# Performance work log

Hardware: AMD Instinct MI355X
Metric: run time of the kernel (lower is better)

## Reference

```python
import jax, jax.numpy as jnp
import numpy as np

GROUPS = 32
EPS = 1e-5


def setup_inputs() -> dict:
    key = jax.random.key(0)
    ks = jax.random.split(key, 8)
    B, C, H, W = 4, 512, 64, 64
    s = 1.0 / np.sqrt(C)  # conv1x1 fan-in init scale
    return {
        "x": jax.random.normal(ks[0], (B, C, H, W), dtype=jnp.float32),
        "gn_gamma": jnp.ones((C,), dtype=jnp.float32),
        "gn_beta": jnp.zeros((C,), dtype=jnp.float32),
        "wq": jax.random.normal(ks[1], (C, C), dtype=jnp.float32) * s,
        "bq": jnp.zeros((C,), dtype=jnp.float32),
        "wk": jax.random.normal(ks[2], (C, C), dtype=jnp.float32) * s,
        "bk": jnp.zeros((C,), dtype=jnp.float32),
        "wv": jax.random.normal(ks[3], (C, C), dtype=jnp.float32) * s,
        "bv": jnp.zeros((C,), dtype=jnp.float32),
    }


def reference(x, gn_gamma, gn_beta, wq, bq, wk, bk, wv, bv):
    B, C, H, W = x.shape
    N = H * W
    # GroupNorm over (channels-within-group, H, W)
    xg = x.reshape(B, GROUPS, C // GROUPS, H, W)
    mean = xg.mean(axis=(2, 3, 4), keepdims=True)
    var = xg.var(axis=(2, 3, 4), keepdims=True)
    xn = ((xg - mean) * jax.lax.rsqrt(var + EPS)).reshape(B, C, H, W)
    xn = xn * gn_gamma[None, :, None, None] + gn_beta[None, :, None, None]
    # 1x1 convs as channel matmuls over flattened spatial tokens: (B, C, N)
    xf = xn.reshape(B, C, N)
    q = jnp.einsum("oc,bcn->bon", wq, xf) + bq[None, :, None]  # (B, Co, N)
    k = jnp.einsum("oc,bcn->bon", wk, xf) + bk[None, :, None]
    v = jnp.einsum("oc,bcn->bon", wv, xf) + bv[None, :, None]
    # scores[b, m, n] = <Q_m, K_n> / sqrt(Co); full N x N matrix as in original
    scale = 1.0 / jnp.sqrt(jnp.asarray(C, dtype=x.dtype))
    scores = jnp.einsum("bcm,bcn->bmn", q, k) * scale  # (B, N, N)
    prob = jax.nn.softmax(scores, axis=-1)
    # out[b, c, m] = sum_n prob[b, m, n] * v[b, c, n]
    attn = jnp.einsum("bmn,bcn->bcm", prob, v).reshape(B, C, H, W)
    return x + attn  # ResLine is Identity since ch_in == ch_out
```

## Files before the change

kernel.cpp:

```cpp
#include <hip/hip_runtime.h>
#include <cstdint>

typedef __attribute__((ext_vector_type(8))) short short8;
typedef __attribute__((ext_vector_type(4))) float floatx4;
typedef __attribute__((ext_vector_type(8))) int intx8;

__device__ __forceinline__ unsigned short f2bf(float f) {
  unsigned int u = __float_as_uint(f);
  u += 0x7fffu + ((u >> 16) & 1u);
  return (unsigned short)(u >> 16);
}

__global__ __launch_bounds__(256) void gn_partial_kernel(
    const float* __restrict__ x, float* __restrict__ gsums) {
  const int b = blockIdx.x >> 8;
  const int g = (blockIdx.x >> 3) & 31;
  const int e = blockIdx.x & 7;
  const long long off = ((long long)(b * 512 + g * 16)) * 4096;
  const float4* xp = (const float4*)(x + off) + e * 2048;
  float s = 0.f, ss = 0.f;
  for (int i = threadIdx.x; i < 2048; i += 256) {
    float4 v = xp[i];
    s  += v.x + v.y + v.z + v.w;
    ss += v.x * v.x + v.y * v.y + v.z * v.z + v.w * v.w;
  }
  for (int off2 = 32; off2; off2 >>= 1) { s += __shfl_down(s, off2); ss += __shfl_down(ss, off2); }
  __shared__ float sb[8];
  const int lane = threadIdx.x & 63, wave = threadIdx.x >> 6;
  if (lane == 0) { sb[wave] = s; sb[4 + wave] = ss; }
  __syncthreads();
  if (threadIdx.x == 0) {
    atomicAdd(gsums + (b * 32 + g) * 2,     sb[0] + sb[1] + sb[2] + sb[3]);
    atomicAdd(gsums + (b * 32 + g) * 2 + 1, sb[4] + sb[5] + sb[6] + sb[7]);
  }
}

__global__ __launch_bounds__(256) void gn_finalize_kernel(
    const float* __restrict__ gsums, const float* __restrict__ gamma,
    const float* __restrict__ beta, float* __restrict__ scale,
    float* __restrict__ shift) {
  const int i = blockIdx.x * 256 + threadIdx.x;
  const int b = i >> 9;
  const int c = i & 511;
  const int g = c >> 4;
  const float S  = gsums[(b * 32 + g) * 2];
  const float SS = gsums[(b * 32 + g) * 2 + 1];
  const float mean = S * (1.f / 65536.f);
  const float var  = SS * (1.f / 65536.f) - mean * mean;
  const float inv  = rsqrtf(var + 1e-5f);
  const float sc = gamma[c] * inv;
  scale[i] = sc;
  shift[i] = beta[c] - mean * sc;
}

__global__ __launch_bounds__(256) void wcvt_zero_kernel(
    const float* __restrict__ wq, const float* __restrict__ wk,
    const float* __restrict__ wv, unsigned short* __restrict__ w16,
    float* __restrict__ zp, int nzero) {
  const int gi = blockIdx.x * 256 + threadIdx.x;
  if (gi < 196608) {
    const int m = gi >> 16;
    const int i = gi & 65535;
    const float* src = (m == 0) ? wq : (m == 1) ? wk : wv;
    float4 v = *((const float4*)src + i);
    ushort4 o;
    o.x = f2bf(v.x); o.y = f2bf(v.y); o.z = f2bf(v.z); o.w = f2bf(v.w);
    *((ushort4*)(w16 + (long long)m * 262144) + i) = o;
  } else {
    const int zi = gi - 196608;
    if (zi < nzero) zp[zi] = 0.f;
  }
}

__global__ __launch_bounds__(256) void norm_transpose_kernel(
    const float* __restrict__ x, const float* __restrict__ scale,
    const float* __restrict__ shift, unsigned short* __restrict__ xnt) {
  const int b = blockIdx.z;
  const int n0 = blockIdx.x * 64;
  const int c0 = blockIdx.y * 64;
  const int t = threadIdx.x;
  __shared__ unsigned short tile[64][65];
  {
    const int cl = t >> 2;
    const int nc = (t & 3) * 16;
    const int c = c0 + cl;
    const float* xp = x + ((long long)b * 512 + c) * 4096 + n0 + nc;
    const float sc = scale[b * 512 + c];
    const float sh = shift[b * 512 + c];
#pragma unroll
    for (int j = 0; j < 16; j += 4) {
      float4 v = *(const float4*)(xp + j);
      tile[cl][nc + j + 0] = f2bf(v.x * sc + sh);
      tile[cl][nc + j + 1] = f2bf(v.y * sc + sh);
      tile[cl][nc + j + 2] = f2bf(v.z * sc + sh);
      tile[cl][nc + j + 3] = f2bf(v.w * sc + sh);
    }
  }
  __syncthreads();
  {
    const int nl = t >> 2;
    const int cc = (t & 3) * 16;
    union { unsigned short u[16]; uint4 q[2]; } o;
#pragma unroll
    for (int j = 0; j < 16; ++j) o.u[j] = tile[cc + j][nl];
    unsigned short* op = xnt + ((long long)b * 4096 + n0 + nl) * 512 + c0 + cc;
    *((uint4*)op) = o.q[0];
    *((uint4*)op + 1) = o.q[1];
  }
}

__global__ __launch_bounds__(256) void zero_kernel(float* __restrict__ p, int n) {
  const int i = blockIdx.x * 256 + threadIdx.x;
  if (i < n) p[i] = 0.f;
}

template <int EPI>
__global__ __launch_bounds__(256) void gemm_tn_kernel(
    const unsigned short* __restrict__ A, const unsigned short* __restrict__ B,
    void* __restrict__ C, const float* __restrict__ bias,
    const float* __restrict__ bias2,
    int lda, int ldb, int ldc, int K,
    long long sA, long long sB, long long sC) {
  const int tid = threadIdx.x;
  const int lane = tid & 63;
  const int wave = tid >> 6;
  const int m0 = blockIdx.x * 128;
  const int n0 = blockIdx.y * 128;
  const int bz = blockIdx.z;
  A += (long long)bz * sA;
  B += (long long)bz * sB;

  __shared__ unsigned short smem[17408];
  unsigned short* As = smem;
  unsigned short* Bs = smem + 8192;

  floatx4 acc[4][4];
#pragma unroll
  for (int i = 0; i < 4; ++i)
#pragma unroll
    for (int j = 0; j < 4; ++j) acc[i][j] = (floatx4){0.f, 0.f, 0.f, 0.f};

  const unsigned short* ag[4];
  const unsigned short* bg[4];
  unsigned ldsoff[4];
#pragma unroll
  for (int i = 0; i < 4; ++i) {
    const int idx = i * 256 + tid;
    const int r = idx >> 3;
    const int g = idx & 7;
    const int gs = g ^ (r & 7);
    ag[i] = A + (long long)(m0 + r) * lda + gs * 8;
    bg[i] = B + (long long)(n0 + r) * ldb + gs * 8;
    ldsoff[i] = (unsigned)(i * 256 + wave * 64) * 8;
  }

  const int l15 = lane & 15;
  const int wm = (wave >> 1) * 64;
  const int wn = (wave & 1) * 64;

  for (int k0 = 0; k0 < K; k0 += 64) {
#pragma unroll
    for (int i = 0; i < 4; ++i) {
      __builtin_amdgcn_global_load_lds(
          (const __attribute__((address_space(1))) void*)(ag[i] + k0),
          (__attribute__((address_space(3))) void*)(As + ldsoff[i]), 16, 0, 0);
      __builtin_amdgcn_global_load_lds(
          (const __attribute__((address_space(1))) void*)(bg[i] + k0),
          (__attribute__((address_space(3))) void*)(Bs + ldsoff[i]), 16, 0, 0);
    }
    __syncthreads();
#pragma unroll
    for (int kk = 0; kk < 64; kk += 32) {
      const int gq = (kk >> 3) + (lane >> 4);
      short8 af[4], bfr[4];
#pragma unroll
      for (int mt = 0; mt < 4; ++mt) {
        const int row = wm + mt * 16 + l15;
        af[mt] = *(const short8*)&As[row * 64 + ((gq ^ (row & 7)) << 3)];
      }
#pragma unroll
      for (int nt = 0; nt < 4; ++nt) {
        const int row = wn + nt * 16 + l15;
        bfr[nt] = *(const short8*)&Bs[row * 64 + ((gq ^ (row & 7)) << 3)];
      }
#pragma unroll
      for (int mt = 0; mt < 4; ++mt)
#pragma unroll
        for (int nt = 0; nt < 4; ++nt)
          acc[mt][nt] = __builtin_amdgcn_mfma_f32_16x16x32_bf16(
              af[mt], bfr[nt], acc[mt][nt], 0, 0, 0);
    }
    __syncthreads();
  }

  const int r0 = (lane >> 4) * 4;

  if (EPI == 6) {
    unsigned char* t8 = (unsigned char*)smem;
    const float* bp = (m0 >= 512) ? bias2 : bias;
    const int mb = m0 & 511;
#pragma unroll
    for (int mt = 0; mt < 4; ++mt) {
      const int ml = wm + mt * 16 + r0;
      const float b0 = bp[mb + ml], b1 = bp[mb + ml + 1];
      const float b2 = bp[mb + ml + 2], b3 = bp[mb + ml + 3];
      const int gw = ml >> 4;
      const int mby = ml & 15;
#pragma unroll
      for (int nt = 0; nt < 4; ++nt) {
        const int nl = wn + nt * 16 + l15;
        int p = __builtin_amdgcn_cvt_pk_fp8_f32(acc[mt][nt][0] + b0,
                                                acc[mt][nt][1] + b1, 0, false);
        p = __builtin_amdgcn_cvt_pk_fp8_f32(acc[mt][nt][2] + b2,
                                            acc[mt][nt][3] + b3, p, true);
        *(int*)&t8[nl * 128 + ((gw ^ (nl & 7)) << 4) + mby] = p;
      }
    }
    __syncthreads();
    unsigned char* o8 = (unsigned char*)C + (long long)bz * sC;
#pragma unroll
    for (int t = 0; t < 4; ++t) {
      const int gid = t * 256 + tid;
      const int row = gid >> 3;
      const int gc = gid & 7;
      uint4 v = *(const uint4*)&t8[row * 128 + ((gc ^ (row & 7)) << 4)];
      *(uint4*)&o8[(long long)(n0 + row) * ldc + m0 + gc * 16] = v;
    }
    return;
  }

#pragma unroll
  for (int mt = 0; mt < 4; ++mt) {
#pragma unroll
    for (int nt = 0; nt < 4; ++nt) {
      const int nl = wn + nt * 16 + l15;
#pragma unroll
      for (int r = 0; r < 4; ++r) {
        const int ml = wm + mt * 16 + r0 + r;
        smem[ml * 136 + nl] = f2bf(acc[mt][nt][r] + bias[m0 + ml]);
      }
    }
  }
  __syncthreads();
  {
    unsigned short* o = (unsigned short*)C + (long long)bz * sC;
#pragma unroll
    for (int j = 0; j < 8; ++j) {
      const int gid = j * 256 + tid;
      const int m = gid >> 4;
      const int gc = gid & 15;
      short8 v = *(const short8*)&smem[m * 136 + gc * 8];
      *(short8*)&o[(long long)(m0 + m) * ldc + n0 + gc * 8] = v;
    }
  }
}

__global__ __launch_bounds__(256) void sgemm_fp8_kernel(
    const unsigned char* __restrict__ A, const unsigned char* __restrict__ B,
    unsigned short* __restrict__ S, float* __restrict__ lsum,
    long long sA, long long sB, long long sC, long long sL) {
  const int tid = threadIdx.x;
  const int lane = tid & 63;
  const int wave = tid >> 6;
  const int quad = lane >> 4;
  const int l15 = lane & 15;
  const int j0 = blockIdx.x * 128;
  const int i0 = blockIdx.y * 128;
  const int bz = blockIdx.z;
  A += (long long)bz * sA;
  B += (long long)bz * sB;

  __shared__ unsigned short smem[17408];
  unsigned char* As = (unsigned char*)smem;
  unsigned char* Bs = (unsigned char*)smem + 16384;

  floatx4 acc[4][4];
#pragma unroll
  for (int i = 0; i < 4; ++i)
#pragma unroll
    for (int j = 0; j < 4; ++j) acc[i][j] = (floatx4){0.f, 0.f, 0.f, 0.f};

  const unsigned char* ag[4];
  const unsigned char* bg[4];
  unsigned ldsoff[4];
#pragma unroll
  for (int i = 0; i < 4; ++i) {
    const int idx = i * 256 + tid;
    const int r = idx >> 3;
    const int g = idx & 7;
    const int gs = g ^ (r & 7);
    ag[i] = A + (long long)(j0 + r) * 1024 + gs * 16;
    bg[i] = B + (long long)(i0 + r) * 1024 + gs * 16;
    ldsoff[i] = (unsigned)(i * 256 + wave * 64) * 16;
  }

  const int wj = (wave >> 1) * 64;
  const int wi = (wave & 1) * 64;

  for (int k0 = 0; k0 < 512; k0 += 128) {
#pragma unroll
    for (int i = 0; i < 4; ++i) {
      __builtin_amdgcn_global_load_lds(
          (const __attribute__((address_space(1))) void*)(ag[i] + k0),
          (__attribute__((address_space(3))) void*)(As + ldsoff[i]), 16, 0, 0);
      __builtin_amdgcn_global_load_lds(
          (const __attribute__((address_space(1))) void*)(bg[i] + k0),
          (__attribute__((address_space(3))) void*)(Bs + ldsoff[i]), 16, 0, 0);
    }
    __syncthreads();
    intx8 af[4], bq[4];
#pragma unroll
    for (int t = 0; t < 4; ++t) {
      {
        const int row = wj + t * 16 + l15;
        const int r7 = row & 7;
        const uint4 x0 = *(const uint4*)(As + row * 128 + (((2 * quad) ^ r7) << 4));
        const uint4 x1 = *(const uint4*)(As + row * 128 + (((2 * quad + 1) ^ r7) << 4));
        af[t] = (intx8){(int)x0.x, (int)x0.y, (int)x0.z, (int)x0.w,
                        (int)x1.x, (int)x1.y, (int)x1.z, (int)x1.w};
      }
      {
        const int row = wi + t * 16 + l15;
        const int r7 = row & 7;
        const uint4 x0 = *(const uint4*)(Bs + row * 128 + (((2 * quad) ^ r7) << 4));
        const uint4 x1 = *(const uint4*)(Bs + row * 128 + (((2 * quad + 1) ^ r7) << 4));
        bq[t] = (intx8){(int)x0.x, (int)x0.y, (int)x0.z, (int)x0.w,
                        (int)x1.x, (int)x1.y, (int)x1.z, (int)x1.w};
      }
    }
#pragma unroll
    for (int jt = 0; jt < 4; ++jt)
#pragma unroll
      for (int it = 0; it < 4; ++it)
        acc[jt][it] = __builtin_amdgcn_mfma_scale_f32_16x16x128_f8f6f4(
            af[jt], bq[it], acc[jt][it], 0, 0, 0, 127, 0, 127);
    __syncthreads();
  }

  const float SCL = 0.044194173824159216f;
  const int jr = quad * 4;
  float rs_it[4] = {0.f, 0.f, 0.f, 0.f};
#pragma unroll
  for (int jt = 0; jt < 4; ++jt) {
#pragma unroll
    for (int it = 0; it < 4; ++it) {
      const int il = wi + it * 16 + l15;
      const int jl = wj + jt * 16 + jr;
      unsigned long long pk = 0;
#pragma unroll
      for (int r = 0; r < 4; ++r) {
        const float e = __expf(acc[jt][it][r] * SCL);
        rs_it[it] += e;
        pk |= (unsigned long long)(__float_as_uint(e) >> 16) << (16 * r);
      }
      *(unsigned long long*)&smem[il * 136 + jl] = pk;
    }
  }
  float* lrow = lsum + (long long)bz * sL;
#pragma unroll
  for (int it = 0; it < 4; ++it) {
    float rs = rs_it[it];
    rs += __shfl_xor(rs, 16);
    rs += __shfl_xor(rs, 32);
    if (quad == 0) atomicAdd(lrow + i0 + wi + it * 16 + l15, rs);
  }
  __syncthreads();
  unsigned short* o = S + (long long)bz * sC;
#pragma unroll
  for (int t = 0; t < 8; ++t) {
    const int gid = t * 256 + tid;
    const int row = gid >> 4;
    const int gc = gid & 15;
    short8 v = *(const short8*)&smem[row * 136 + gc * 8];
    *(short8*)&o[(long long)(i0 + row) * 4096 + j0 + gc * 8] = v;
  }
}

__global__ __launch_bounds__(256) void pv_kernel(
    const unsigned short* __restrict__ A,
    const unsigned short* __restrict__ B,
    float* __restrict__ out, const float* __restrict__ res,
    const float* __restrict__ lsum,
    long long sA, long long sB, long long sC, long long sL) {
  const int id = blockIdx.x;
  const int xcd = id & 7;
  const int slot = id >> 3;
  const int m0 = (slot & 3) * 128;
  const int grp = xcd + 8 * (slot >> 2);
  const int n0 = (grp & 31) * 128;
  const int bz = grp >> 5;
  A += (long long)bz * sA;
  B += (long long)bz * sB;

  const int tid = threadIdx.x;
  const int lane = tid & 63;
  const int wave = tid >> 6;

  __shared__ unsigned short As[8192];
  __shared__ unsigned short Bs[8192];

  floatx4 acc[4][4];
#pragma unroll
  for (int i = 0; i < 4; ++i)
#pragma unroll
    for (int j = 0; j < 4; ++j) acc[i][j] = (floatx4){0.f, 0.f, 0.f, 0.f};

  const unsigned short* ag[4];
  const unsigned short* bg[4];
  unsigned ldsoff[4];
#pragma unroll
  for (int i = 0; i < 4; ++i) {
    const int idx = i * 256 + tid;
    const int r = idx >> 3;
    const int g = idx & 7;
    const int gs = g ^ (r & 7);
    ag[i] = A + (long long)(m0 + r) * 4096 + gs * 8;
    bg[i] = B + (long long)(n0 + r) * 4096 + gs * 8;
    ldsoff[i] = (unsigned)(i * 256 + wave * 64) * 8;
  }

  const int l15 = lane & 15;
  const int wm = (wave >> 1) * 64;
  const int wn = (wave & 1) * 64;

  for (int k0 = 0; k0 < 4096; k0 += 64) {
#pragma unroll
    for (int i = 0; i < 4; ++i) {
      __builtin_amdgcn_global_load_lds(
          (const __attribute__((address_space(1))) void*)(ag[i] + k0),
          (__attribute__((address_space(3))) void*)(As + ldsoff[i]), 16, 0, 0);
      __builtin_amdgcn_global_load_lds(
          (const __attribute__((address_space(1))) void*)(bg[i] + k0),
          (__attribute__((address_space(3))) void*)(Bs + ldsoff[i]), 16, 0, 0);
    }
    __syncthreads();
#pragma unroll
    for (int kk = 0; kk < 64; kk += 32) {
      const int gq = (kk >> 3) + (lane >> 4);
      short8 af[4], bfr[4];
#pragma unroll
      for (int mt = 0; mt < 4; ++mt) {
        const int row = wm + mt * 16 + l15;
        af[mt] = *(const short8*)&As[row * 64 + ((gq ^ (row & 7)) << 3)];
      }
#pragma unroll
      for (int nt = 0; nt < 4; ++nt) {
        const int row = wn + nt * 16 + l15;
        bfr[nt] = *(const short8*)&Bs[row * 64 + ((gq ^ (row & 7)) << 3)];
      }
#pragma unroll
      for (int mt = 0; mt < 4; ++mt)
#pragma unroll
        for (int nt = 0; nt < 4; ++nt)
          acc[mt][nt] = __builtin_amdgcn_mfma_f32_16x16x32_bf16(
              af[mt], bfr[nt], acc[mt][nt], 0, 0, 0);
    }
    __syncthreads();
  }

  const int r0 = (lane >> 4) * 4;
  float* o = out + (long long)bz * sC;
  const float* rr = res + (long long)bz * sC;
  const float* lrow = lsum + (long long)bz * sL;
#pragma unroll
  for (int mt = 0; mt < 4; ++mt) {
#pragma unroll
    for (int nt = 0; nt < 4; ++nt) {
      const int n = n0 + wn + nt * 16 + l15;
      const float inv = 1.f / lrow[n];
#pragma unroll
      for (int r = 0; r < 4; ++r) {
        const int m = m0 + wm + mt * 16 + r0 + r;
        const long long off = (long long)m * 4096 + n;
        o[off] = acc[mt][nt][r] * inv + rr[off];
      }
    }
  }
}

extern "C" void kernel_launch(void* const* d_in, const int* in_sizes, int n_in,
                              void* d_out, int out_size, void* d_ws, size_t ws_size,
                              hipStream_t stream) {
  const float* x     = (const float*)d_in[0];
  const float* gamma = (const float*)d_in[1];
  const float* beta  = (const float*)d_in[2];
  const float* wq    = (const float*)d_in[3];
  const float* bq    = (const float*)d_in[4];
  const float* wk    = (const float*)d_in[5];
  const float* bk    = (const float*)d_in[6];
  const float* wv    = (const float*)d_in[7];
  const float* bv    = (const float*)d_in[8];
  float* out = (float*)d_out;

  const long long sTok = 4096LL * 512;
  const long long sQK8 = 4096LL * 1024;
  const long long sS   = 4096LL * 4096;

  char* ws = (char*)d_ws;
  float* scale = (float*)ws;
  float* shift = (float*)(ws + 8192);
  unsigned short* w16 = (unsigned short*)(ws + 16384);
  unsigned short* xnt = (unsigned short*)(ws + 1589248);
  unsigned char*  qk8 = (unsigned char*)(ws + 18366464);
  unsigned short* vv  = (unsigned short*)(ws + 51920896);

  const bool full = ws_size >= 202982400ULL;

  float* lsum;
  int nzero;
  if (full) {
    lsum = (float*)(ws + 202915840);
    nzero = 16384 + 256;
  } else {
    lsum = (float*)(ws + 102252544);
    nzero = 4096 + 256;
  }
  float* gsums = lsum + nzero - 256;

  wcvt_zero_kernel<<<768 + (nzero + 255) / 256, 256, 0, stream>>>(
      wq, wk, wv, w16, lsum, nzero);
  gn_partial_kernel<<<1024, 256, 0, stream>>>(x, gsums);
  gn_finalize_kernel<<<8, 256, 0, stream>>>(gsums, gamma, beta, scale, shift);
  norm_transpose_kernel<<<dim3(64, 8, 4), 256, 0, stream>>>(x, scale, shift, xnt);

  gemm_tn_kernel<6><<<dim3(8, 32, 4), 256, 0, stream>>>(
      w16, xnt, qk8, bq, bk, 512, 512, 1024, 512, 0, sTok, sQK8);
  gemm_tn_kernel<2><<<dim3(4, 32, 4), 256, 0, stream>>>(
      w16 + 524288, xnt, vv, bv, nullptr, 512, 512, 4096, 512, 0, sTok, sTok);

  if (full) {
    unsigned short* S = (unsigned short*)(ws + 68698112);
    sgemm_fp8_kernel<<<dim3(32, 32, 4), 256, 0, stream>>>(
        qk8 + 512, qk8, S, lsum, sQK8, sQK8, sS, 4096);
    pv_kernel<<<512, 256, 0, stream>>>(
        vv, S, out, x, lsum, sTok, sS, sTok, 4096);
  } else {
    unsigned short* S = (unsigned short*)(ws + 68698112);
    for (int b = 0; b < 4; ++b) {
      if (b) zero_kernel<<<16, 256, 0, stream>>>(lsum, 4096);
      sgemm_fp8_kernel<<<dim3(32, 32, 1), 256, 0, stream>>>(
          qk8 + (long long)b * sQK8 + 512, qk8 + (long long)b * sQK8, S, lsum,
          0, 0, 0, 0);
      pv_kernel<<<128, 256, 0, stream>>>(
          vv + (long long)b * sTok, S, out + (long long)b * sTok,
          x + (long long)b * sTok, lsum, 0, 0, 0, 0);
    }
  }
}
```

Before: 288.3 us.

## Triple-buffer PV GEMM with 512-thread 128x256 tiles and interleaved async loads

Reworks the PV kernel to use 512-thread blocks, each computing a 128x256 output tile. Global-to-LDS loads are triple-buffered, issued two stages ahead and split across the two k-halves, with explicit vmcnt waits, raw barriers and raised priority around the MFMA bursts. The aim is to hide global load latency behind matrix math and raise reuse of the A tile, at the cost of much larger LDS use (144KB) and fewer blocks in flight. The reciprocal of the row sums is also hoisted out of the epilogue loop.

```diff
diff --git a/kernel.cpp b/kernel.cpp
--- a/kernel.cpp
+++ b/kernel.cpp
@@ -376,7 +376,34 @@
   }
 }
 
-__global__ __launch_bounds__(256) void pv_kernel(
+__device__ __forceinline__ void pv_ld_frags(
+    const unsigned short* As, const unsigned short* Bs, int kk, int lane,
+    int wm, int wn, short8* af, short8* bf) {
+  const int l15 = lane & 15;
+  const int gq = (kk >> 3) + (lane >> 4);
+#pragma unroll
+  for (int mt = 0; mt < 4; ++mt) {
+    const int row = wm + mt * 16 + l15;
+    af[mt] = *(const short8*)&As[row * 64 + ((gq ^ (row & 7)) << 3)];
+  }
+#pragma unroll
+  for (int nt = 0; nt < 4; ++nt) {
+    const int row = wn + nt * 16 + l15;
+    bf[nt] = *(const short8*)&Bs[row * 64 + ((gq ^ (row & 7)) << 3)];
+  }
+}
+
+__device__ __forceinline__ void pv_mfma(const short8* af, const short8* bf,
+                                        floatx4 (&acc)[4][4]) {
+#pragma unroll
+  for (int mt = 0; mt < 4; ++mt)
+#pragma unroll
+    for (int nt = 0; nt < 4; ++nt)
+      acc[mt][nt] = __builtin_amdgcn_mfma_f32_16x16x32_bf16(
+          af[mt], bf[nt], acc[mt][nt], 0, 0, 0);
+}
+
+__global__ __launch_bounds__(512, 2) void pv_kernel(
     const unsigned short* __restrict__ A,
     const unsigned short* __restrict__ B,
     float* __restrict__ out, const float* __restrict__ res,
@@ -387,17 +414,19 @@
   const int slot = id >> 3;
   const int m0 = (slot & 3) * 128;
   const int grp = xcd + 8 * (slot >> 2);
-  const int n0 = (grp & 31) * 128;
-  const int bz = grp >> 5;
+  const int n0 = (grp & 15) * 256;
+  const int bz = grp >> 4;
   A += (long long)bz * sA;
   B += (long long)bz * sB;
 
   const int tid = threadIdx.x;
   const int lane = tid & 63;
   const int wave = tid >> 6;
-
-  __shared__ unsigned short As[8192];
-  __shared__ unsigned short Bs[8192];
+  const int l15 = lane & 15;
+  const int wm = (wave >> 2) * 64;
+  const int wn = (wave & 3) * 64;
+
+  __shared__ unsigned short smem[73728];
 
   floatx4 acc[4][4];
 #pragma unroll
@@ -405,74 +434,112 @@
 #pragma unroll
     for (int j = 0; j < 4; ++j) acc[i][j] = (floatx4){0.f, 0.f, 0.f, 0.f};
 
-  const unsigned short* ag[4];
+  const unsigned short* ag[2];
   const unsigned short* bg[4];
-  unsigned ldsoff[4];
-#pragma unroll
-  for (int i = 0; i < 4; ++i) {
-    const int idx = i * 256 + tid;
+  unsigned ao[2], bo[4];
+#pragma unroll
+  for (int j = 0; j < 2; ++j) {
+    const int idx = j * 512 + tid;
     const int r = idx >> 3;
     const int g = idx & 7;
-    const int gs = g ^ (r & 7);
-    ag[i] = A + (long long)(m0 + r) * 4096 + gs * 8;
-    bg[i] = B + (long long)(n0 + r) * 4096 + gs * 8;
-    ldsoff[i] = (unsigned)(i * 256 + wave * 64) * 8;
-  }
-
-  const int l15 = lane & 15;
-  const int wm = (wave >> 1) * 64;
-  const int wn = (wave & 1) * 64;
-
-  for (int k0 = 0; k0 < 4096; k0 += 64) {
-#pragma unroll
-    for (int i = 0; i < 4; ++i) {
-      __builtin_amdgcn_global_load_lds(
-          (const __attribute__((address_space(1))) void*)(ag[i] + k0),
-          (__attribute__((address_space(3))) void*)(As + ldsoff[i]), 16, 0, 0);
-      __builtin_amdgcn_global_load_lds(
-          (const __attribute__((address_space(1))) void*)(bg[i] + k0),
-          (__attribute__((address_space(3))) void*)(Bs + ldsoff[i]), 16, 0, 0);
-    }
-    __syncthreads();
-#pragma unroll
-    for (int kk = 0; kk < 64; kk += 32) {
-      const int gq = (kk >> 3) + (lane >> 4);
-      short8 af[4], bfr[4];
-#pragma unroll
-      for (int mt = 0; mt < 4; ++mt) {
-        const int row = wm + mt * 16 + l15;
-        af[mt] = *(const short8*)&As[row * 64 + ((gq ^ (row & 7)) << 3)];
-      }
-#pragma unroll
-      for (int nt = 0; nt < 4; ++nt) {
-        const int row = wn + nt * 16 + l15;
-        bfr[nt] = *(const short8*)&Bs[row * 64 + ((gq ^ (row & 7)) << 3)];
-      }
-#pragma unroll
-      for (int mt = 0; mt < 4; ++mt)
-#pragma unroll
-        for (int nt = 0; nt < 4; ++nt)
-          acc[mt][nt] = __builtin_amdgcn_mfma_f32_16x16x32_bf16(
-              af[mt], bfr[nt], acc[mt][nt], 0, 0, 0);
-    }
-    __syncthreads();
-  }
+    ag[j] = A + (long long)(m0 + r) * 4096 + ((g ^ (r & 7)) << 3);
+    ao[j] = (unsigned)(j * 512 + wave * 64) * 8;
+  }
+#pragma unroll
+  for (int j = 0; j < 4; ++j) {
+    const int idx = j * 512 + tid;
+    const int r = idx >> 3;
+    const int g = idx & 7;
+    bg[j] = B + (long long)(n0 + r) * 4096 + ((g ^ (r & 7)) << 3);
+    bo[j] = 8192u + (unsigned)(j * 512 + wave * 64) * 8;
+  }
+
+#define PV_GLDS(gp, lp)                                              \
+  __builtin_amdgcn_global_load_lds(                                  \
+      (const __attribute__((address_space(1))) void*)(gp),           \
+      (__attribute__((address_space(3))) void*)(lp), 16, 0, 0)
+#define PV_STA(tt, base)                                             \
+  {                                                                  \
+    PV_GLDS(ag[0] + (tt) * 64, smem + (base) + ao[0]);               \
+    PV_GLDS(ag[1] + (tt) * 64, smem + (base) + ao[1]);               \
+    PV_GLDS(bg[0] + (tt) * 64, smem + (base) + bo[0]);               \
+  }
+#define PV_STB(tt, base)                                             \
+  {                                                                  \
+    PV_GLDS(bg[1] + (tt) * 64, smem + (base) + bo[1]);               \
+    PV_GLDS(bg[2] + (tt) * 64, smem + (base) + bo[2]);               \
+    PV_GLDS(bg[3] + (tt) * 64, smem + (base) + bo[3]);               \
+  }
+#define PV_BAR()                                                     \
+  {                                                                  \
+    asm volatile("" ::: "memory");                                   \
+    __builtin_amdgcn_s_barrier();                                    \
+    asm volatile("" ::: "memory");                                   \
+  }
+
+  PV_STA(0, 0); PV_STB(0, 0);
+  PV_STA(1, 24576); PV_STB(1, 24576);
+  asm volatile("s_waitcnt vmcnt(6)" ::: "memory");
+  PV_BAR();
+
+  int cur = 0;
+  for (int t = 0; t < 64; ++t) {
+    const unsigned short* As = smem + cur * 24576;
+    const unsigned short* Bs = As + 8192;
+    const int nb = (cur == 0) ? 2 : cur - 1;
+    const int nbase = nb * 24576;
+    const bool st = (t < 62);
+    short8 af[4], bf[4];
+
+    pv_ld_frags(As, Bs, 0, lane, wm, wn, af, bf);
+    if (st) PV_STA(t + 2, nbase);
+    PV_BAR();
+    asm volatile("s_waitcnt lgkmcnt(0)" ::: "memory");
+    __builtin_amdgcn_sched_barrier(0);
+    __builtin_amdgcn_s_setprio(1);
+    pv_mfma(af, bf, acc);
+    __builtin_amdgcn_s_setprio(0);
+    PV_BAR();
+
+    pv_ld_frags(As, Bs, 32, lane, wm, wn, af, bf);
+    if (st) {
+      PV_STB(t + 2, nbase);
+      asm volatile("s_waitcnt vmcnt(6)" ::: "memory");
+    } else {
+      asm volatile("s_waitcnt vmcnt(0)" ::: "memory");
+    }
+    PV_BAR();
+    asm volatile("s_waitcnt lgkmcnt(0)" ::: "memory");
+    __builtin_amdgcn_sched_barrier(0);
+    __builtin_amdgcn_s_setprio(1);
+    pv_mfma(af, bf, acc);
+    __builtin_amdgcn_s_setprio(0);
+    PV_BAR();
+
+    cur = (cur == 2) ? 0 : cur + 1;
+  }
+#undef PV_GLDS
+#undef PV_STA
+#undef PV_STB
+#undef PV_BAR
 
   const int r0 = (lane >> 4) * 4;
   float* o = out + (long long)bz * sC;
   const float* rr = res + (long long)bz * sC;
   const float* lrow = lsum + (long long)bz * sL;
+  float inv[4];
+#pragma unroll
+  for (int nt = 0; nt < 4; ++nt) inv[nt] = 1.f / lrow[n0 + wn + nt * 16 + l15];
 #pragma unroll
   for (int mt = 0; mt < 4; ++mt) {
 #pragma unroll
     for (int nt = 0; nt < 4; ++nt) {
       const int n = n0 + wn + nt * 16 + l15;
-      const float inv = 1.f / lrow[n];
 #pragma unroll
       for (int r = 0; r < 4; ++r) {
         const int m = m0 + wm + mt * 16 + r0 + r;
         const long long off = (long long)m * 4096 + n;
-        o[off] = acc[mt][nt][r] * inv + rr[off];
+        o[off] = acc[mt][nt][r] * inv[nt] + rr[off];
       }
     }
   }
@@ -532,7 +599,7 @@
     unsigned short* S = (unsigned short*)(ws + 68698112);
     sgemm_fp8_kernel<<<dim3(32, 32, 4), 256, 0, stream>>>(
         qk8 + 512, qk8, S, lsum, sQK8, sQK8, sS, 4096);
-    pv_kernel<<<512, 256, 0, stream>>>(
+    pv_kernel<<<256, 512, 0, stream>>>(
         vv, S, out, x, lsum, sTok, sS, sTok, 4096);
   } else {
     unsigned short* S = (unsigned short*)(ws + 68698112);
@@ -541,7 +608,7 @@
       sgemm_fp8_kernel<<<dim3(32, 32, 1), 256, 0, stream>>>(
           qk8 + (long long)b * sQK8 + 512, qk8 + (long long)b * sQK8, S, lsum,
           0, 0, 0, 0);
-      pv_kernel<<<128, 256, 0, stream>>>(
+      pv_kernel<<<64, 512, 0, stream>>>(
           vv + (long long)b * sTok, S, out + (long long)b * sTok,
           x + (long long)b * sTok, lsum, 0, 0, 0, 0);
     }
```

Result: no change. 285.6 us (-0.9%).
